# Performance work log

Measured on AMD Instinct MI355X. Metric: run time of the kernel, lower is better.

Reference implementation:

```python
import jax, jax.numpy as jnp
import numpy as np

B, L, C, H = 2, 2048, 1024, 16
D = C // H
THETA = 50000.0


def rotate_half(x):
    x1, x2 = jnp.split(x, 2, axis=-1)
    return jnp.concatenate((-x2, x1), axis=-1)


def rope_freqs(n, dim):
    inv_freq = 1.0 / (THETA ** (jnp.arange(0, dim, 2, dtype=jnp.float32) / dim))
    freqs = jnp.arange(n, dtype=jnp.float32)[:, None] * inv_freq[None, :]  # [n, dim//2]
    return jnp.concatenate((freqs, freqs), axis=-1)  # [n, dim]


def setup_inputs() -> dict:
    key = jax.random.key(0)
    ks = jax.random.split(key, 8)
    q = jax.random.normal(ks[0], (B, L, C), dtype=jnp.float32)
    mask = jax.random.randint(ks[1], (B, L), 0, 2) > 0
    mask = mask.at[:, 0].set(True)  # avoid fully-masked rows
    s = 1.0 / np.sqrt(C)
    Wq = jax.random.normal(ks[2], (C, C), dtype=jnp.float32) * s
    Wk = jax.random.normal(ks[3], (C, C), dtype=jnp.float32) * s
    Wv = jax.random.normal(ks[4], (C, C), dtype=jnp.float32) * s
    Wo = jax.random.normal(ks[5], (C, C), dtype=jnp.float32) * s
    bo = jnp.zeros((C,), dtype=jnp.float32)
    return {"q": q, "mask": mask, "Wq": Wq, "Wk": Wk, "Wv": Wv, "Wo": Wo, "bo": bo}


def reference(q, mask, Wq, Wk, Wv, Wo, bo):
    x = q
    # QKV projections (torch Linear: y = x @ W.T)
    def proj(W):
        y = jnp.einsum('blc,oc->blo', x, W)
        return y.reshape(B, L, H, D).transpose(0, 2, 1, 3)  # [B,H,L,D]
    qh, kh, vh = proj(Wq), proj(Wk), proj(Wv)
    # RoPE (L == S)
    pos = rope_freqs(L, D)  # [L, D]
    cos, sin = jnp.cos(pos), jnp.sin(pos)
    qh = qh * cos + rotate_half(qh) * sin
    kh = kh * cos + rotate_half(kh) * sin
    # masked SDPA with additive bias (-inf where mask is False)
    scale = 1.0 / np.sqrt(D)
    bias = jnp.where(mask[:, None, None, :], 0.0, -jnp.inf)  # [B,1,1,S]
    scores = jnp.einsum('bhld,bhsd->bhls', qh, kh) * scale + bias
    attn = jax.nn.softmax(scores, axis=-1)
    out = jnp.einsum('bhls,bhsd->bhld', attn, vh)
    out = out.transpose(0, 2, 1, 3).reshape(B, L, C)
    return jnp.einsum('blc,oc->blo', out, Wo) + bo
```

## Files before the change

kernel.cpp:

```cpp
#include <hip/hip_runtime.h>
#include <hip/hip_bf16.h>

typedef __hip_bfloat16 bf16;
typedef short bf16x8 __attribute__((ext_vector_type(8)));
typedef short bf16x4 __attribute__((ext_vector_type(4)));
typedef float floatx4 __attribute__((ext_vector_type(4)));

#define Bb 2
#define Ll 2048
#define Cc 1024
#define Hh 16
#define Dd 64
#define INVFREQ_LN 0.3381180763f
#define QSCALE 0.1803368801f
#define NCONV 4096

#define GLD16(gp, lp) __builtin_amdgcn_global_load_lds( \
    (const __attribute__((address_space(1))) void*)(gp), \
    (__attribute__((address_space(3))) void*)(lp), 16, 0, 0)

__device__ inline short f2bf(float f) {
    __hip_bfloat16 h = __float2bfloat16(f);
    return *reinterpret_cast<short*>(&h);
}
__device__ inline short f2bf_rn(float f) {
    return (short)((__float_as_uint(f) + 0x8000u) >> 16);
}
__device__ inline int cvtpk_bf16(float lo, float hi) {
    int r;
    asm("v_cvt_pk_bf16_f32 %0, %1, %2" : "=v"(r) : "v"(lo), "v"(hi));
    return r;
}
__device__ inline float exp2_fast(float x) {
    float r;
    asm("v_exp_f32 %0, %1" : "=v"(r) : "v"(x));
    return r;
}

__global__ __launch_bounds__(256) void convert_scan(
    const float* __restrict__ x, const float* __restrict__ wq,
    const float* __restrict__ wk, const float* __restrict__ wv,
    const float* __restrict__ wo,
    bf16* __restrict__ xb, bf16* __restrict__ wqkv, bf16* __restrict__ wob,
    const int* __restrict__ mask, int* __restrict__ cidx, int* __restrict__ valid)
{
    if (blockIdx.x >= NCONV) {
        const int b   = blockIdx.x - NCONV;
        const int tid = threadIdx.x;
        const int base = b * Ll + tid * 8;
        int m[8]; int s = 0;
        #pragma unroll
        for (int i = 0; i < 8; i++) { m[i] = mask[base + i] ? 1 : 0; s += m[i]; }
        const int lane = tid & 63;
        int xx = s;
        #pragma unroll
        for (int off = 1; off < 64; off <<= 1) {
            int y = __shfl_up(xx, off);
            if (lane >= off) xx += y;
        }
        __shared__ int wtot[4];
        if (lane == 63) wtot[tid >> 6] = xx;
        __syncthreads();
        int wbase = 0;
        const int w = tid >> 6;
        #pragma unroll
        for (int i = 0; i < 4; i++) if (i < w) wbase += wtot[i];
        int run = wbase + (xx - s);
        #pragma unroll
        for (int i = 0; i < 8; i++) { cidx[base + i] = run; run += m[i]; }
        if (tid == 255) valid[b] = run;
        return;
    }

    const int XN = (Bb * Ll * Cc) / 8;
    const int WN = (Cc * Cc) / 8;
    int i = blockIdx.x * 256 + threadIdx.x;
    const float* src; bf16* dst;
    if (i < XN)               { src = x  + (size_t)i * 8;                 dst = xb   + (size_t)i * 8; }
    else if (i < XN + WN)     { int j = i - XN;        src = wq + (size_t)j * 8; dst = wqkv + (size_t)j * 8; }
    else if (i < XN + 2*WN)   { int j = i - XN - WN;   src = wk + (size_t)j * 8; dst = wqkv + (size_t)Cc*Cc     + (size_t)j * 8; }
    else if (i < XN + 3*WN)   { int j = i - XN - 2*WN; src = wv + (size_t)j * 8; dst = wqkv + (size_t)Cc*Cc*2   + (size_t)j * 8; }
    else                      { int j = i - XN - 3*WN; src = wo + (size_t)j * 8; dst = wob  + (size_t)j * 8; }
    float4 a = *reinterpret_cast<const float4*>(src);
    float4 b = *reinterpret_cast<const float4*>(src + 4);
    float vv[8] = {a.x, a.y, a.z, a.w, b.x, b.y, b.z, b.w};
    bf16x8 o;
    #pragma unroll
    for (int t = 0; t < 8; t++) o[t] = f2bf(vv[t]);
    *reinterpret_cast<bf16x8*>(dst) = o;
}

template <int ROWS, int NTHREADS>
__device__ __forceinline__ void stage_swz(const bf16* __restrict__ g, int ldk,
                                          short* lds, int tid)
{
    #pragma unroll
    for (int s = 0; s < (ROWS * 4) / NTHREADS; s++) {
        const int idx = s * NTHREADS + tid;
        const int r   = idx >> 2;
        const int col = ((idx & 3) ^ ((r >> 1) & 3)) << 3;
        GLD16(g + (size_t)r * ldk + col, lds + idx * 8);
    }
}

#define VMCNT(N) asm volatile("s_waitcnt vmcnt(" #N ")" ::: "memory")

__global__ __launch_bounds__(256, 3) void gemm_qkv(
    const bf16* __restrict__ A, const bf16* __restrict__ W,
    bf16* __restrict__ qb, bf16* __restrict__ kb, bf16* __restrict__ vb,
    const int* __restrict__ cmask, const int* __restrict__ cidx)
{
    constexpr int K = Cc;
    constexpr int T = K / 32;

    __shared__ __align__(16) short As[3][128 * 32];
    __shared__ __align__(16) short Bs[3][128 * 32];

    const int tid  = threadIdx.x;
    const int wave = tid >> 6;
    const int lane = tid & 63;
    const int l15  = lane & 15;
    const int quad = lane >> 4;
    const int wm   = wave >> 1;
    const int wn   = wave & 1;

    const int lin = blockIdx.y * 24 + blockIdx.x;
    const int swz = (lin & 7) * 96 + (lin >> 3);
    const int m0  = (swz / 24) * 128;
    const int n0  = (swz % 24) * 128;

    const bf16* Ag = A + (size_t)m0 * K;
    const bf16* Wg = W + (size_t)n0 * K;

    const int gsw = (quad ^ ((l15 >> 1) & 3)) << 3;

    floatx4 acc[4][4];
    #pragma unroll
    for (int mt = 0; mt < 4; mt++)
        #pragma unroll
        for (int nt = 0; nt < 4; nt++)
            #pragma unroll
            for (int r = 0; r < 4; r++) acc[mt][nt][r] = 0.f;

    stage_swz<128, 256>(Ag,      K, &As[0][0], tid);
    stage_swz<128, 256>(Wg,      K, &Bs[0][0], tid);
    stage_swz<128, 256>(Ag + 32, K, &As[1][0], tid);
    stage_swz<128, 256>(Wg + 32, K, &Bs[1][0], tid);
    VMCNT(4);
    __builtin_amdgcn_s_barrier();

    int cur = 0;
    for (int t = 0; t < T; t++) {
        const short* Ac = &As[0][0] + cur * (128 * 32);
        const short* Bc = &Bs[0][0] + cur * (128 * 32);

        if (t + 2 < T) {
            int nb = cur + 2; if (nb >= 3) nb -= 3;
            const int kk = (t + 2) << 5;
            stage_swz<128, 256>(Ag + kk, K, &As[nb][0], tid);
            stage_swz<128, 256>(Wg + kk, K, &Bs[nb][0], tid);
        }

        bf16x8 af[4], bfr[4];
        #pragma unroll
        for (int nt = 0; nt < 4; nt++)
            bfr[nt] = *(const bf16x8*)(Bc + (wn * 64 + nt * 16 + l15) * 32 + gsw);
        #pragma unroll
        for (int mt = 0; mt < 4; mt++)
            af[mt] = *(const bf16x8*)(Ac + (wm * 64 + mt * 16 + l15) * 32 + gsw);

        #pragma unroll
        for (int mt = 0; mt < 4; mt++)
            #pragma unroll
            for (int nt = 0; nt < 4; nt++)
                acc[mt][nt] = __builtin_amdgcn_mfma_f32_16x16x32_bf16(
                    af[mt], bfr[nt], acc[mt][nt], 0, 0, 0);

        if (t + 2 < T) { VMCNT(4); }
        else           { VMCNT(0); }
        __builtin_amdgcn_s_barrier();

        cur++; if (cur == 3) cur = 0;
    }

    const int colbase = n0 + wn * 64;
    const int which   = colbase >> 10;
    const int hh      = (colbase & (Cc - 1)) >> 6;
    if (which == 2) {
        #pragma unroll
        for (int mt = 0; mt < 4; mt++)
            #pragma unroll
            for (int r = 0; r < 4; r++) {
                int row = m0 + wm * 64 + mt * 16 + quad * 4 + r;
                int b = row >> 11, l = row & (Ll - 1);
                if (cmask[b * Ll + l]) {
                    int c = cidx[b * Ll + l];
                    size_t head = (size_t)(b * Hh + hh) * Dd * Ll;
                    int lbase = (c & ~63) | (c & 7);
                    int lg    = (c >> 3) & 7;
                    #pragma unroll
                    for (int nt = 0; nt < 4; nt++) {
                        int d = nt * 16 + l15;
                        int pos = lbase | ((lg ^ (d & 7)) << 3);
                        vb[head + (size_t)d * Ll + pos] = __float2bfloat16(acc[mt][nt][r]);
                    }
                }
            }
    } else {
        bf16* dst = which ? kb : qb;
        const float qs = which ? 1.0f : QSCALE;
        const float base0 = __expf(-(float)l15 * INVFREQ_LN);
        const float base1 = __expf(-(float)(l15 + 16) * INVFREQ_LN);
        #pragma unroll
        for (int mt = 0; mt < 4; mt++)
            #pragma unroll
            for (int r = 0; r < 4; r++) {
                int row = m0 + wm * 64 + mt * 16 + quad * 4 + r;
                int b = row >> 11, l = row & (Ll - 1);
                int cm = 1, c = l;
                if (which == 1) {
                    cm = cmask[b * Ll + l];
                    c  = cidx[b * Ll + l];
                }
                if (cm) {
                    size_t rb = ((size_t)(b * Hh + hh) * Ll + c) * Dd;
                    #pragma unroll
                    for (int nt2 = 0; nt2 < 2; nt2++) {
                        float fr = (float)l * (nt2 ? base1 : base0);
                        float sn, cs;
                        __sincosf(fr, &sn, &cs);
                        float x1 = acc[mt][nt2][r];
                        float x2 = acc[mt][nt2 + 2][r];
                        float o1 = (x1 * cs - x2 * sn) * qs;
                        float o2 = (x2 * cs + x1 * sn) * qs;
                        int d1 = nt2 * 16 + l15;
                        int d2 = d1 + 32;
                        if (which == 1) {
                            int sw = c & 7;
                            int a1 = ((((d1 >> 3) ^ sw)) << 3) | (d1 & 7);
                            int a2 = ((((d2 >> 3) ^ sw)) << 3) | (d2 & 7);
                            dst[rb + a1] = __float2bfloat16(o1);
                            dst[rb + a2] = __float2bfloat16(o2);
                        } else {
                            dst[rb + d1] = __float2bfloat16(o1);
                            dst[rb + d2] = __float2bfloat16(o2);
                        }
                    }
                }
            }
    }
}

__global__ __launch_bounds__(256, 4) void gemm_out(
    const bf16* __restrict__ A, const bf16* __restrict__ W,
    float* __restrict__ outf, const float* __restrict__ bias)
{
    constexpr int K = Cc, N = Cc;
    constexpr int T = K / 32;

    __shared__ __align__(16) short As[3][64 * 32];
    __shared__ __align__(16) short Bs[3][64 * 32];

    const int tid  = threadIdx.x;
    const int wave = tid >> 6;
    const int lane = tid & 63;
    const int l15  = lane & 15;
    const int quad = lane >> 4;
    const int wm   = wave >> 1;
    const int wn   = wave & 1;

    const int lin = blockIdx.y * 16 + blockIdx.x;
    const int swz = (lin & 7) * 128 + (lin >> 3);
    const int m0  = (swz >> 4) * 64;
    const int n0  = (swz & 15) * 64;

    const bf16* Ag = A + (size_t)m0 * K;
    const bf16* Wg = W + (size_t)n0 * K;

    const int gsw = (quad ^ ((l15 >> 1) & 3)) << 3;

    floatx4 acc[2][2];
    #pragma unroll
    for (int mt = 0; mt < 2; mt++)
        #pragma unroll
        for (int nt = 0; nt < 2; nt++)
            #pragma unroll
            for (int r = 0; r < 4; r++) acc[mt][nt][r] = 0.f;

    stage_swz<64, 256>(Ag,      K, &As[0][0], tid);
    stage_swz<64, 256>(Wg,      K, &Bs[0][0], tid);
    stage_swz<64, 256>(Ag + 32, K, &As[1][0], tid);
    stage_swz<64, 256>(Wg + 32, K, &Bs[1][0], tid);
    VMCNT(2);
    __builtin_amdgcn_s_barrier();

    int cur = 0;
    for (int t = 0; t < T; t++) {
        const short* Ac = &As[0][0] + cur * (64 * 32);
        const short* Bc = &Bs[0][0] + cur * (64 * 32);

        if (t + 2 < T) {
            int nb = cur + 2; if (nb >= 3) nb -= 3;
            const int kk = (t + 2) << 5;
            stage_swz<64, 256>(Ag + kk, K, &As[nb][0], tid);
            stage_swz<64, 256>(Wg + kk, K, &Bs[nb][0], tid);
        }

        bf16x8 af[2], bfr[2];
        #pragma unroll
        for (int mt = 0; mt < 2; mt++)
            af[mt] = *(const bf16x8*)(Ac + (wm * 32 + mt * 16 + l15) * 32 + gsw);
        #pragma unroll
        for (int nt = 0; nt < 2; nt++)
            bfr[nt] = *(const bf16x8*)(Bc + (wn * 32 + nt * 16 + l15) * 32 + gsw);

        #pragma unroll
        for (int mt = 0; mt < 2; mt++)
            #pragma unroll
            for (int nt = 0; nt < 2; nt++)
                acc[mt][nt] = __builtin_amdgcn_mfma_f32_16x16x32_bf16(
                    af[mt], bfr[nt], acc[mt][nt], 0, 0, 0);

        if (t + 2 < T) { VMCNT(2); }
        else           { VMCNT(0); }
        __builtin_amdgcn_s_barrier();

        cur++; if (cur == 3) cur = 0;
    }

    #pragma unroll
    for (int mt = 0; mt < 2; mt++)
        #pragma unroll
        for (int r = 0; r < 4; r++) {
            int row = m0 + wm * 32 + mt * 16 + quad * 4 + r;
            #pragma unroll
            for (int nt = 0; nt < 2; nt++) {
                int col = n0 + wn * 32 + nt * 16 + l15;
                outf[(size_t)row * N + col] = acc[mt][nt][r] + bias[col];
            }
        }
}

#define KVB 128

__global__ __launch_bounds__(512) void attn_mfma(
    const bf16* __restrict__ q, const bf16* __restrict__ k, const bf16* __restrict__ vt,
    const int* __restrict__ valid, bf16* __restrict__ ctx)
{
    __shared__ __align__(16) short Ks[2][KVB * 64];
    __shared__ __align__(16) short Vs[2][KVB * 64];
    __shared__ __align__(16) short Ps[8][16 * 64];

    const int tid  = threadIdx.x;
    const int wave = tid >> 6;
    const int lane = tid & 63;
    const int l15  = lane & 15;
    const int quad = lane >> 4;

    const int bh = blockIdx.x & 31;
    const int q0 = (blockIdx.x >> 5) << 7;
    const int b  = bh >> 4;
    const int h  = bh & (Hh - 1);

    const int nvalid = valid[b];
    const int ntiles = (nvalid + KVB - 1) >> 7;

    const short* qb  = (const short*)(q  + (size_t)bh * Ll * Dd);
    const short* kb  = (const short*)(k  + (size_t)bh * Ll * Dd);
    const short* vtb = (const short*)(vt + (size_t)bh * Dd * Ll);

    const int qrow = q0 + wave * 16 + l15;
    bf16x8 qa0 = *(const bf16x8*)(qb + (size_t)qrow * Dd + quad * 8);
    bf16x8 qa1 = *(const bf16x8*)(qb + (size_t)qrow * Dd + 32 + quad * 8);

    const int g0 = ((quad ^ (l15 & 7)) << 3);
    const int g1 = (((quad + 4) ^ (l15 & 7)) << 3);

    const short* vgp = vtb + (size_t)(tid >> 3) * Ll + ((tid & 7) << 3);
    short* ksl = &Ks[0][0] + tid * 8;
    short* vsl = &Vs[0][0] + tid * 8;
    const int lbuf = KVB * 64;

    floatx4 O[4];
    float l_r = 0.f;
    #pragma unroll
    for (int nt = 0; nt < 4; nt++)
        #pragma unroll
        for (int r = 0; r < 4; r++) O[nt][r] = 0.f;

    GLD16(kb + tid * 8,        ksl);
    GLD16(kb + 4096 + tid * 8, ksl + 4096);
    GLD16(vgp,                 vsl);
    GLD16(vgp + 64,            vsl + 4096);

    short* Pw = &Ps[wave][0];

    for (int t = 0; t < ntiles; t++) {
        const int cur = t & 1;
        __builtin_amdgcn_s_barrier();
        if (t + 1 < ntiles) {
            const size_t s1 = (size_t)(t + 1) * KVB;
            GLD16(kb + s1 * 64 + tid * 8,        ksl + (cur ^ 1) * lbuf);
            GLD16(kb + s1 * 64 + 4096 + tid * 8, ksl + (cur ^ 1) * lbuf + 4096);
            GLD16(vgp + s1,                      vsl + (cur ^ 1) * lbuf);
            GLD16(vgp + s1 + 64,                 vsl + (cur ^ 1) * lbuf + 4096);
            VMCNT(4);
        } else {
            VMCNT(0);
        }

        const short* Kc = &Ks[cur][0];
        const short* Vc = &Vs[cur][0];

        #pragma unroll
        for (int c = 0; c < 2; c++) {
            floatx4 S[4];
            #pragma unroll
            for (int nt = 0; nt < 4; nt++) {
                const short* krow = Kc + (c * 64 + nt * 16 + l15) * 64;
                bf16x8 ka0 = *(const bf16x8*)(krow + g0);
                bf16x8 ka1 = *(const bf16x8*)(krow + g1);
                floatx4 acc; acc[0] = acc[1] = acc[2] = acc[3] = 0.f;
                acc = __builtin_amdgcn_mfma_f32_16x16x32_bf16(ka0, qa0, acc, 0, 0, 0);
                acc = __builtin_amdgcn_mfma_f32_16x16x32_bf16(ka1, qa1, acc, 0, 0, 0);
                S[nt] = acc;
            }

            const int kglob0 = t * KVB + c * 64;
            if (kglob0 + 64 <= nvalid) {
                #pragma unroll
                for (int nt = 0; nt < 4; nt++) {
                    float p0 = exp2_fast(S[nt][0]);
                    float p1 = exp2_fast(S[nt][1]);
                    float p2 = exp2_fast(S[nt][2]);
                    float p3 = exp2_fast(S[nt][3]);
                    l_r += (p0 + p1) + (p2 + p3);
                    int2 pw;
                    pw.x = cvtpk_bf16(p0, p1);
                    pw.y = cvtpk_bf16(p2, p3);
                    int grp = (2 * nt + (quad >> 1)) ^ (l15 & 7);
                    *(int2*)&Pw[l15 * 64 + (grp << 3) + ((quad & 1) << 2)] = pw;
                }
            } else {
                const int kb0 = kglob0 + quad * 4;
                #pragma unroll
                for (int nt = 0; nt < 4; nt++) {
                    float p[4];
                    #pragma unroll
                    for (int r = 0; r < 4; r++) {
                        p[r] = (kb0 + nt * 16 + r < nvalid) ? exp2_fast(S[nt][r]) : 0.f;
                        l_r += p[r];
                    }
                    int2 pw;
                    pw.x = cvtpk_bf16(p[0], p[1]);
                    pw.y = cvtpk_bf16(p[2], p[3]);
                    int grp = (2 * nt + (quad >> 1)) ^ (l15 & 7);
                    *(int2*)&Pw[l15 * 64 + (grp << 3) + ((quad & 1) << 2)] = pw;
                }
            }

            bf16x8 pb0 = *(const bf16x8*)&Pw[l15 * 64 + ((quad ^ (l15 & 7)) << 3)];
            bf16x8 pb1 = *(const bf16x8*)&Pw[l15 * 64 + (((4 + quad) ^ (l15 & 7)) << 3)];
            #pragma unroll
            for (int nt = 0; nt < 4; nt++) {
                const short* vrow = Vc + c * 4096 + (nt * 16 + l15) * 64;
                bf16x8 va0 = *(const bf16x8*)(vrow + g0);
                bf16x8 va1 = *(const bf16x8*)(vrow + g1);
                O[nt] = __builtin_amdgcn_mfma_f32_16x16x32_bf16(va0, pb0, O[nt], 0, 0, 0);
                O[nt] = __builtin_amdgcn_mfma_f32_16x16x32_bf16(va1, pb1, O[nt], 0, 0, 0);
            }
        }
    }

    float l = l_r;
    l += __shfl_xor(l, 16);
    l += __shfl_xor(l, 32);
    const float inv = 1.0f / l;

    {
        int row = q0 + wave * 16 + l15;
        short* cp = (short*)ctx + ((size_t)(b * Ll + row)) * Cc + h * Dd;
        #pragma unroll
        for (int nt = 0; nt < 4; nt++) {
            int2 ov;
            ov.x = cvtpk_bf16(O[nt][0] * inv, O[nt][1] * inv);
            ov.y = cvtpk_bf16(O[nt][2] * inv, O[nt][3] * inv);
            *(int2*)&cp[nt * 16 + quad * 4] = ov;
        }
    }
}

extern "C" void kernel_launch(void* const* d_in, const int* in_sizes, int n_in,
                              void* d_out, int out_size, void* d_ws, size_t ws_size,
                              hipStream_t stream) {
    const float* x    = (const float*)d_in[0];
    const int*   mask = (const int*)d_in[1];
    const float* Wq   = (const float*)d_in[2];
    const float* Wk   = (const float*)d_in[3];
    const float* Wv   = (const float*)d_in[4];
    const float* Wo   = (const float*)d_in[5];
    const float* bo   = (const float*)d_in[6];
    float* out = (float*)d_out;

    const size_t per = (size_t)Bb * Hh * Ll * Dd;
    bf16* qbuf = (bf16*)d_ws;
    bf16* kbuf = qbuf + per;
    bf16* vbuf = kbuf + per;
    bf16* xb   = vbuf + per;
    bf16* wqkv = xb + per;
    bf16* wob  = wqkv + (size_t)3 * Cc * Cc;
    int*  cidx   = (int*)(wob + (size_t)Cc * Cc);
    int*  cvalid = cidx + Bb * Ll;
    bf16* ctx  = xb;

    const int M = Bb * Ll;

    convert_scan<<<NCONV + Bb, 256, 0, stream>>>(
        x, Wq, Wk, Wv, Wo, xb, wqkv, wob, mask, cidx, cvalid);

    dim3 gQKV(3 * Cc / 128, M / 128);
    gemm_qkv<<<gQKV, 256, 0, stream>>>(xb, wqkv, qbuf, kbuf, vbuf, mask, cidx);

    attn_mfma<<<Bb * Hh * (Ll / 128), 512, 0, stream>>>(qbuf, kbuf, vbuf, cvalid, ctx);

    dim3 gOut(Cc / 64, M / 64);
    gemm_out<<<gOut, 256, 0, stream>>>(ctx, wob, out, bo);
}
```

Baseline: 171.5 us.

## Gather only unmasked rows for K/V projection and skip fully-masked tiles

The mask scan now builds an inverse index from compacted positions to original rows. The QKV GEMM gathers A rows through this index for K/V column tiles and returns early for tiles past the valid count. About half the K/V projection work is skipped, since roughly half the mask is false. In exchange, A loads become per-row gathers through pointers, and the gather index plus early-return logic add complexity.

```diff
diff --git a/kernel.cpp b/kernel.cpp
--- a/kernel.cpp
+++ b/kernel.cpp
@@ -42,7 +42,7 @@
     const float* __restrict__ wk, const float* __restrict__ wv,
     const float* __restrict__ wo,
     bf16* __restrict__ xb, bf16* __restrict__ wqkv, bf16* __restrict__ wob,
-    const int* __restrict__ mask, int* __restrict__ cidx, int* __restrict__ valid)
+    const int* __restrict__ mask, int* __restrict__ inv, int* __restrict__ valid)
 {
     if (blockIdx.x >= NCONV) {
         const int b   = blockIdx.x - NCONV;
@@ -67,7 +67,10 @@
         for (int i = 0; i < 4; i++) if (i < w) wbase += wtot[i];
         int run = wbase + (xx - s);
         #pragma unroll
-        for (int i = 0; i < 8; i++) { cidx[base + i] = run; run += m[i]; }
+        for (int i = 0; i < 8; i++) {
+            if (m[i]) inv[b * Ll + run] = tid * 8 + i;
+            run += m[i];
+        }
         if (tid == 255) valid[b] = run;
         return;
     }
@@ -103,12 +106,29 @@
     }
 }
 
+__device__ __forceinline__ void stage_rows2(const bf16* rp0, const bf16* rp1, int kk,
+                                            short* lds, int tid)
+{
+    {
+        const int idx = tid;
+        const int r   = idx >> 2;
+        const int col = ((idx & 3) ^ ((r >> 1) & 3)) << 3;
+        GLD16(rp0 + kk + col, lds + idx * 8);
+    }
+    {
+        const int idx = 256 + tid;
+        const int r   = idx >> 2;
+        const int col = ((idx & 3) ^ ((r >> 1) & 3)) << 3;
+        GLD16(rp1 + kk + col, lds + idx * 8);
+    }
+}
+
 #define VMCNT(N) asm volatile("s_waitcnt vmcnt(" #N ")" ::: "memory")
 
 __global__ __launch_bounds__(256, 3) void gemm_qkv(
     const bf16* __restrict__ A, const bf16* __restrict__ W,
     bf16* __restrict__ qb, bf16* __restrict__ kb, bf16* __restrict__ vb,
-    const int* __restrict__ cmask, const int* __restrict__ cidx)
+    const int* __restrict__ valid, const int* __restrict__ inv)
 {
     constexpr int K = Cc;
     constexpr int T = K / 32;
@@ -129,7 +149,30 @@
     const int m0  = (swz / 24) * 128;
     const int n0  = (swz % 24) * 128;
 
-    const bf16* Ag = A + (size_t)m0 * K;
+    const int isKV = (n0 >= Cc);
+    const int b    = m0 >> 11;
+    const int c0   = m0 & (Ll - 1);
+    int nvb = Ll;
+    if (isKV) {
+        nvb = valid[b];
+        if (c0 >= nvb) return;
+    }
+
+    const bf16* rp0;
+    const bf16* rp1;
+    {
+        const int r1 = tid >> 2;
+        const int r2 = 64 + (tid >> 2);
+        if (isKV) {
+            int l1 = (c0 + r1 < nvb) ? inv[b * Ll + c0 + r1] : 0;
+            int l2 = (c0 + r2 < nvb) ? inv[b * Ll + c0 + r2] : 0;
+            rp0 = A + (size_t)(b * Ll + l1) * K;
+            rp1 = A + (size_t)(b * Ll + l2) * K;
+        } else {
+            rp0 = A + (size_t)(m0 + r1) * K;
+            rp1 = A + (size_t)(m0 + r2) * K;
+        }
+    }
     const bf16* Wg = W + (size_t)n0 * K;
 
     const int gsw = (quad ^ ((l15 >> 1) & 3)) << 3;
@@ -142,9 +185,9 @@
             #pragma unroll
             for (int r = 0; r < 4; r++) acc[mt][nt][r] = 0.f;
 
-    stage_swz<128, 256>(Ag,      K, &As[0][0], tid);
+    stage_rows2(rp0, rp1, 0,  &As[0][0], tid);
     stage_swz<128, 256>(Wg,      K, &Bs[0][0], tid);
-    stage_swz<128, 256>(Ag + 32, K, &As[1][0], tid);
+    stage_rows2(rp0, rp1, 32, &As[1][0], tid);
     stage_swz<128, 256>(Wg + 32, K, &Bs[1][0], tid);
     VMCNT(4);
     __builtin_amdgcn_s_barrier();
@@ -157,7 +200,7 @@
         if (t + 2 < T) {
             int nb = cur + 2; if (nb >= 3) nb -= 3;
             const int kk = (t + 2) << 5;
-            stage_swz<128, 256>(Ag + kk, K, &As[nb][0], tid);
+            stage_rows2(rp0, rp1, kk, &As[nb][0], tid);
             stage_swz<128, 256>(Wg + kk, K, &Bs[nb][0], tid);
         }
 
@@ -192,9 +235,8 @@
             #pragma unroll
             for (int r = 0; r < 4; r++) {
                 int row = m0 + wm * 64 + mt * 16 + quad * 4 + r;
-                int b = row >> 11, l = row & (Ll - 1);
-                if (cmask[b * Ll + l]) {
-                    int c = cidx[b * Ll + l];
+                int c = row & (Ll - 1);
+                if (c < nvb) {
                     size_t head = (size_t)(b * Hh + hh) * Dd * Ll;
                     int lbase = (c & ~63) | (c & 7);
                     int lg    = (c >> 3) & 7;
@@ -216,11 +258,14 @@
             #pragma unroll
             for (int r = 0; r < 4; r++) {
                 int row = m0 + wm * 64 + mt * 16 + quad * 4 + r;
-                int b = row >> 11, l = row & (Ll - 1);
-                int cm = 1, c = l;
+                int c, l, cm = 1;
                 if (which == 1) {
-                    cm = cmask[b * Ll + l];
-                    c  = cidx[b * Ll + l];
+                    c = row & (Ll - 1);
+                    cm = (c < nvb);
+                    l  = cm ? inv[b * Ll + c] : 0;
+                } else {
+                    c = row & (Ll - 1);
+                    l = c;
                 }
                 if (cm) {
                     size_t rb = ((size_t)(b * Hh + hh) * Ll + c) * Dd;
@@ -509,17 +554,17 @@
     bf16* xb   = vbuf + per;
     bf16* wqkv = xb + per;
     bf16* wob  = wqkv + (size_t)3 * Cc * Cc;
-    int*  cidx   = (int*)(wob + (size_t)Cc * Cc);
-    int*  cvalid = cidx + Bb * Ll;
+    int*  inv    = (int*)(wob + (size_t)Cc * Cc);
+    int*  cvalid = inv + Bb * Ll;
     bf16* ctx  = xb;
 
     const int M = Bb * Ll;
 
     convert_scan<<<NCONV + Bb, 256, 0, stream>>>(
-        x, Wq, Wk, Wv, Wo, xb, wqkv, wob, mask, cidx, cvalid);
+        x, Wq, Wk, Wv, Wo, xb, wqkv, wob, mask, inv, cvalid);
 
     dim3 gQKV(3 * Cc / 128, M / 128);
-    gemm_qkv<<<gQKV, 256, 0, stream>>>(xb, wqkv, qbuf, kbuf, vbuf, mask, cidx);
+    gemm_qkv<<<gQKV, 256, 0, stream>>>(xb, wqkv, qbuf, kbuf, vbuf, cvalid, inv);
 
     attn_mfma<<<Bb * Hh * (Ll / 128), 512, 0, stream>>>(qbuf, kbuf, vbuf, cvalid, ctx);
 
```

New measurement: 174.3 us. About the same (+1.6%).
